# Performance work log

Measured on AMD Instinct MI355X. Metric: run time of the kernel, lower is better.

Reference implementation:

```python
import jax, jax.numpy as jnp
import numpy as np

EMBED_DIM = 1024
N_HEAD = 16
D_K = EMBED_DIM // N_HEAD


def setup_inputs() -> dict:
    key = jax.random.key(0)
    kq, kk, kv, kwq, kwk, kwv, kwo = jax.random.split(key, 7)
    B, S, E = 4, 2048, EMBED_DIM
    scale = 1.0 / np.sqrt(E)
    return {
        "Q": jax.random.normal(kq, (B, S, E), dtype=jnp.float32),
        "K": jax.random.normal(kk, (B, S, E), dtype=jnp.float32),
        "V": jax.random.normal(kv, (B, S, E), dtype=jnp.float32),
        "mask": jnp.zeros((1,), dtype=jnp.bool_),  # unused by the module's forward
        "Wq": jax.random.normal(kwq, (E, E), dtype=jnp.float32) * scale,
        "Wk": jax.random.normal(kwk, (E, E), dtype=jnp.float32) * scale,
        "Wv": jax.random.normal(kwv, (E, E), dtype=jnp.float32) * scale,
        "Wo": jax.random.normal(kwo, (E, E), dtype=jnp.float32) * scale,
    }


def reference(Q, K, V, mask, Wq, Wk, Wv, Wo):
    B, S, E = Q.shape
    H, Dk = N_HEAD, D_K
    # Linear projections (torch Linear: x @ W.T), split into heads -> [B,H,S,Dk]
    q = (Q @ Wq.T).reshape(B, S, H, Dk).transpose(0, 2, 1, 3)
    k = (K @ Wk.T).reshape(B, S, H, Dk).transpose(0, 2, 1, 3)
    v = (V @ Wv.T).reshape(B, S, H, Dk).transpose(0, 2, 1, 3)
    # Scaled dot-product attention (no mask is passed in the original forward;
    # dropout is identity in eval mode)
    scores = jnp.einsum("bhqd,bhkd->bhqk", q, k) / jnp.sqrt(jnp.float32(Dk))
    attn = jax.nn.softmax(scores, axis=-1)
    ctx = jnp.einsum("bhqk,bhkd->bhqd", attn, v)  # [B,H,S,Dk]
    ctx = ctx.transpose(0, 2, 1, 3).reshape(B, S, E)
    return ctx @ Wo.T
```

## Files before the change

kernel.cpp:

```cpp
#include <hip/hip_runtime.h>
#include <hip/hip_bf16.h>

#define B_  4
#define S_  2048
#define E_  1024
#define H_  16
#define DK_ 64
#define CSC 0.18033688011112042f

using bf16   = __bf16;
using bf16x8 = __attribute__((ext_vector_type(8))) __bf16;
using f32x4  = __attribute__((ext_vector_type(4))) float;

__device__ __forceinline__ f32x4 mfma16(bf16x8 a, bf16x8 b, f32x4 c) {
    return __builtin_amdgcn_mfma_f32_16x16x32_bf16(a, b, c, 0, 0, 0);
}

__device__ __forceinline__ bf16x8 cvt8(float4 a, float4 b) {
    bf16x8 r;
    r[0] = (bf16)a.x; r[1] = (bf16)a.y; r[2] = (bf16)a.z; r[3] = (bf16)a.w;
    r[4] = (bf16)b.x; r[5] = (bf16)b.y; r[6] = (bf16)b.z; r[7] = (bf16)b.w;
    return r;
}

__device__ __forceinline__ void gl16(const void* g, void* l) {
    __builtin_amdgcn_global_load_lds(
        (const __attribute__((address_space(1))) void*)g,
        (__attribute__((address_space(3))) void*)l, 16, 0, 0);
}

#define SBAR()  __builtin_amdgcn_s_barrier()
#define WV4()  { asm volatile("s_waitcnt vmcnt(4)" ::: "memory");   \
                 __builtin_amdgcn_sched_barrier(0); }
#define WL0()  { asm volatile("s_waitcnt lgkmcnt(0)" ::: "memory"); \
                 __builtin_amdgcn_sched_barrier(0); }

__global__ __launch_bounds__(256) void cvt_pair(const float* __restrict__ a,
                                                const float* __restrict__ b,
                                                bf16* __restrict__ da,
                                                bf16* __restrict__ db) {
    const float* s = blockIdx.y ? b : a;
    bf16* d = blockIdx.y ? db : da;
    const size_t i = (size_t)blockIdx.x * 256 + threadIdx.x;
    const float4 u = ((const float4*)s)[i * 2];
    const float4 v = ((const float4*)s)[i * 2 + 1];
    ((bf16x8*)d)[i] = cvt8(u, v);
}

__global__ __launch_bounds__(256) void cvtw3(const float* __restrict__ a,
                                             const float* __restrict__ b,
                                             const float* __restrict__ c,
                                             bf16* __restrict__ d, float s0) {
    const int y = blockIdx.y;
    const float* s = y == 0 ? a : y == 1 ? b : c;
    const float sc = y == 0 ? s0 : 1.f;
    const size_t i = (size_t)blockIdx.x * 256 + threadIdx.x;
    float4 u = ((const float4*)s)[i * 2];
    float4 v = ((const float4*)s)[i * 2 + 1];
    u.x *= sc; u.y *= sc; u.z *= sc; u.w *= sc;
    v.x *= sc; v.y *= sc; v.z *= sc; v.w *= sc;
    ((bf16x8*)(d + (size_t)y * E_ * E_))[i] = cvt8(u, v);
}

template <int MODE>
__global__ __launch_bounds__(512, 2) void gemm8(
    const bf16* __restrict__ Aq, const bf16* __restrict__ Ak,
    const bf16* __restrict__ Av, const bf16* __restrict__ Wb,
    bf16* __restrict__ qws, bf16* __restrict__ kws, bf16* __restrict__ vtws,
    float* __restrict__ fout, int selbase) {
    extern __shared__ __align__(16) char sm[];

    const int t = threadIdx.x;
    const int lane = t & 63, w = t >> 6;
    const int wm = w >> 2, wn = w & 3;
    const int quad = lane >> 4, l16 = lane & 15;

    int sel, gn;
    if (MODE == 0) {
        sel = selbase + (blockIdx.y >> 2);
        gn = (blockIdx.y & 3) * 256;
    } else {
        sel = 0;
        gn = blockIdx.y * 256;
    }
    const int gm = blockIdx.x * 256;

    const bf16* A = (MODE == 1) ? Aq : (sel == 0 ? Aq : sel == 1 ? Ak : Av);
    const bf16* W = (MODE == 1) ? Wb : Wb + (size_t)sel * E_ * E_;

    const int lr = lane >> 3;
    const int scw = (lane & 7) ^ lr;
    const int s0 = w * 2, s1 = s0 + 1;
    const int arow0 = (s0 >> 3) * 128 + (s0 & 7) * 8;
    const int arow1 = (s1 >> 3) * 128 + (s1 & 7) * 8;
    const int brow0 = (s0 >> 2) * 64 + (s0 & 3) * 8;
    const int brow1 = (s1 >> 2) * 64 + (s1 & 3) * 8;

    const char* gAa0 = (const char*)(A + (size_t)(gm + arow0 + lr) * E_) + scw * 16;
    const char* gAa1 = (const char*)(A + (size_t)(gm + arow1 + lr) * E_) + scw * 16;
    const char* gAb0 = gAa0 + (size_t)64 * E_ * 2;
    const char* gAb1 = gAa1 + (size_t)64 * E_ * 2;
    const char* gBa0 = (const char*)(W + (size_t)(gn + brow0 + lr) * E_) + scw * 16;
    const char* gBa1 = (const char*)(W + (size_t)(gn + brow1 + lr) * E_) + scw * 16;
    const char* gBb0 = gBa0 + (size_t)32 * E_ * 2;
    const char* gBb1 = gBa1 + (size_t)32 * E_ * 2;

#define STG_Aa(nb, kb) { gl16(gAa0 + (kb), sm + (nb) + arow0 * 128);              \
                         gl16(gAa1 + (kb), sm + (nb) + arow1 * 128); }
#define STG_Ab(nb, kb) { gl16(gAb0 + (kb), sm + (nb) + (arow0 + 64) * 128);       \
                         gl16(gAb1 + (kb), sm + (nb) + (arow1 + 64) * 128); }
#define STG_Ba(nb, kb) { gl16(gBa0 + (kb), sm + (nb) + 32768 + brow0 * 128);      \
                         gl16(gBa1 + (kb), sm + (nb) + 32768 + brow1 * 128); }
#define STG_Bb(nb, kb) { gl16(gBb0 + (kb), sm + (nb) + 32768 + (brow0+32) * 128); \
                         gl16(gBb1 + (kb), sm + (nb) + 32768 + (brow1+32) * 128); }

    const int cK0 = ((0 * 4 + quad) ^ (l16 & 7)) * 16;
    const int cK1 = ((1 * 4 + quad) ^ (l16 & 7)) * 16;

    f32x4 acc[8][4];
#pragma unroll
    for (int i = 0; i < 8; ++i)
#pragma unroll
        for (int j = 0; j < 4; ++j) acc[i][j] = f32x4{0.f, 0.f, 0.f, 0.f};

    bf16x8 Af[4][2], Bf[2][2];

#define LDA(cb, MH)                                                            \
    _Pragma("unroll") for (int ml = 0; ml < 4; ++ml) {                         \
        const int rb = (wm * 128 + (MH) * 64 + ml * 16 + l16) * 128;           \
        Af[ml][0] = *(const bf16x8*)(sm + (cb) + rb + cK0);                    \
        Af[ml][1] = *(const bf16x8*)(sm + (cb) + rb + cK1);                    \
    }
#define LDB(cb, NH)                                                            \
    _Pragma("unroll") for (int nl = 0; nl < 2; ++nl) {                         \
        const int rb = (wn * 64 + (NH) * 32 + nl * 16 + l16) * 128;            \
        Bf[nl][0] = *(const bf16x8*)(sm + (cb) + 32768 + rb + cK0);            \
        Bf[nl][1] = *(const bf16x8*)(sm + (cb) + 32768 + rb + cK1);            \
    }
#define MFMAQ(MH, NH)                                                          \
    __builtin_amdgcn_s_setprio(1);                                             \
    _Pragma("unroll") for (int ml = 0; ml < 4; ++ml)                           \
    _Pragma("unroll") for (int nl = 0; nl < 2; ++nl) {                         \
        acc[(MH)*4+ml][(NH)*2+nl] =                                            \
            mfma16(Af[ml][0], Bf[nl][0], acc[(MH)*4+ml][(NH)*2+nl]);           \
        acc[(MH)*4+ml][(NH)*2+nl] =                                            \
            mfma16(Af[ml][1], Bf[nl][1], acc[(MH)*4+ml][(NH)*2+nl]);           \
    }                                                                          \
    __builtin_amdgcn_s_setprio(0);

    STG_Aa(0, 0); STG_Ba(0, 0); STG_Bb(0, 0); STG_Ab(0, 0);
    WV4();
    SBAR();

    for (int kt = 0; kt < 16; ++kt) {
        const size_t cb = (size_t)(kt & 1) * 65536;
        const size_t nb = cb ^ 65536;
        const size_t kb = (size_t)(kt + 1 < 16 ? kt + 1 : 15) * 128;

        LDA(cb, 0); LDB(cb, 0);
        STG_Aa(nb, kb);
        WV4(); SBAR(); WL0();
        MFMAQ(0, 0);
        SBAR();

        LDB(cb, 1);
        STG_Ba(nb, kb);
        WV4(); SBAR(); WL0();
        MFMAQ(0, 1);
        SBAR();

        LDA(cb, 1);
        STG_Bb(nb, kb);
        SBAR(); WL0();
        MFMAQ(1, 1);
        SBAR();

        LDB(cb, 0);
        STG_Ab(nb, kb);
        WV4(); SBAR(); WL0();
        MFMAQ(1, 0);
        SBAR();
    }

#pragma unroll
    for (int mf = 0; mf < 8; ++mf)
#pragma unroll
        for (int nf = 0; nf < 4; ++nf) {
            const int col = gn + wn * 64 + nf * 16 + l16;
            const int row0 = gm + wm * 128 + mf * 16 + quad * 4;
            if (MODE == 1) {
#pragma unroll
                for (int r = 0; r < 4; ++r)
                    fout[(size_t)(row0 + r) * E_ + col] = acc[mf][nf][r];
            } else {
                const int h = col >> 6, d = col & (DK_ - 1);
#pragma unroll
                for (int r = 0; r < 4; ++r) {
                    const int i = row0 + r;
                    const int bb = i >> 11, s = i & (S_ - 1);
                    const float v = acc[mf][nf][r];
                    if (sel == 2)
                        vtws[(((size_t)(bb * H_ + h)) * DK_ + d) * S_ + s] = (bf16)v;
                    else if (sel == 1)
                        kws[(((size_t)(bb * H_ + h)) * S_ + s) * DK_ + d] = (bf16)v;
                    else
                        qws[(((size_t)(bb * H_ + h)) * S_ + s) * DK_ + d] = (bf16)v;
                }
            }
        }
#undef STG_Aa
#undef STG_Ab
#undef STG_Ba
#undef STG_Bb
#undef LDA
#undef LDB
#undef MFMAQ
}

#define PSTR 72
__global__ __launch_bounds__(256) void attn4(const bf16* __restrict__ q,
                                             const bf16* __restrict__ k,
                                             const bf16* __restrict__ vt,
                                             bf16* __restrict__ ctx) {
    __shared__ __align__(16) bf16 sK[64 * 64];
    __shared__ __align__(16) bf16 sV[64 * 64];
    __shared__ __align__(16) bf16 plds[4][32 * PSTR];

    const int t = threadIdx.x;
    const int lane = t & 63, wave = t >> 6;
    const int quad = lane >> 4, l16 = lane & 15;
    const int qb = (blockIdx.x * 4 + wave) * 32;
    const int bh = blockIdx.y;
    const size_t base  = (size_t)bh * S_ * DK_;
    const size_t baseT = (size_t)bh * DK_ * S_;
    bf16* pw = &plds[wave][0];

    const int srow = t >> 2, sc4 = (t & 3) * 16;
    const int cb = (t & 3) * 2, swr = srow & 7;
    const bf16* gK = k + base + (size_t)srow * DK_ + sc4;
    const bf16* gV = vt + baseT + (size_t)srow * S_ + sc4;
    char* wK0 = (char*)sK + srow * 128 + ((cb ^ swr) * 16);
    char* wK1 = (char*)sK + srow * 128 + (((cb + 1) ^ swr) * 16);
    char* wV0 = (char*)sV + srow * 128 + ((cb ^ swr) * 16);
    char* wV1 = (char*)sV + srow * 128 + (((cb + 1) ^ swr) * 16);

    bf16x8 rk[2], rv[2];
    rk[0] = *(const bf16x8*)(gK);
    rk[1] = *(const bf16x8*)(gK + 8);
    rv[0] = *(const bf16x8*)(gV);
    rv[1] = *(const bf16x8*)(gV + 8);

    bf16x8 aQ[2][2];
#pragma unroll
    for (int t2 = 0; t2 < 2; ++t2) {
        const bf16* qp = q + base + (size_t)(qb + t2 * 16 + l16) * DK_ + quad * 8;
        aQ[t2][0] = *(const bf16x8*)(qp);
        aQ[t2][1] = *(const bf16x8*)(qp + 32);
    }

    f32x4 acc[2][4];
    float l_i[2][4];
#pragma unroll
    for (int t2 = 0; t2 < 2; ++t2)
#pragma unroll
        for (int nb = 0; nb < 4; ++nb) {
            acc[t2][nb] = f32x4{0.f, 0.f, 0.f, 0.f};
            l_i[t2][nb] = 0.f;
        }

    for (int kt = 0; kt < S_ / 64; ++kt) {
        __syncthreads();
        *(bf16x8*)wK0 = rk[0];
        *(bf16x8*)wK1 = rk[1];
        *(bf16x8*)wV0 = rv[0];
        *(bf16x8*)wV1 = rv[1];
        __syncthreads();
        if (kt + 1 < S_ / 64) {
            const bf16* nK = gK + (size_t)(kt + 1) * 64 * DK_;
            const bf16* nV = gV + (size_t)(kt + 1) * 64;
            rk[0] = *(const bf16x8*)(nK);
            rk[1] = *(const bf16x8*)(nK + 8);
            rv[0] = *(const bf16x8*)(nV);
            rv[1] = *(const bf16x8*)(nV + 8);
        }

        f32x4 sc[2][4];
#pragma unroll
        for (int kb = 0; kb < 4; ++kb) {
            const int r = kb * 16 + l16, sw = r & 7;
            const bf16x8 b0 =
                *(const bf16x8*)((const char*)sK + r * 128 + ((quad ^ sw) * 16));
            const bf16x8 b1 = *(const bf16x8*)((const char*)sK + r * 128 +
                                               (((quad + 4) ^ sw) * 16));
#pragma unroll
            for (int t2 = 0; t2 < 2; ++t2) {
                f32x4 z = f32x4{0.f, 0.f, 0.f, 0.f};
                z = mfma16(aQ[t2][0], b0, z);
                sc[t2][kb] = mfma16(aQ[t2][1], b1, z);
            }
        }

#pragma unroll
        for (int t2 = 0; t2 < 2; ++t2)
#pragma unroll
            for (int r = 0; r < 4; ++r) {
                const int prow = (t2 * 16 + quad * 4 + r) * PSTR;
#pragma unroll
                for (int kb = 0; kb < 4; ++kb) {
                    const float p = __builtin_amdgcn_exp2f(sc[t2][kb][r]);
                    l_i[t2][r] += p;
                    pw[prow + kb * 16 + l16] = (bf16)p;
                }
            }

        bf16x8 aP[2][2];
#pragma unroll
        for (int t2 = 0; t2 < 2; ++t2) {
            aP[t2][0] = *(const bf16x8*)(pw + (t2 * 16 + l16) * PSTR + quad * 8);
            aP[t2][1] = *(const bf16x8*)(pw + (t2 * 16 + l16) * PSTR + 32 + quad * 8);
        }

#pragma unroll
        for (int nb = 0; nb < 4; ++nb) {
            const int r = nb * 16 + l16, sw = r & 7;
            const bf16x8 b0 =
                *(const bf16x8*)((const char*)sV + r * 128 + ((quad ^ sw) * 16));
            const bf16x8 b1 = *(const bf16x8*)((const char*)sV + r * 128 +
                                               (((quad + 4) ^ sw) * 16));
#pragma unroll
            for (int t2 = 0; t2 < 2; ++t2) {
                acc[t2][nb] = mfma16(aP[t2][0], b0, acc[t2][nb]);
                acc[t2][nb] = mfma16(aP[t2][1], b1, acc[t2][nb]);
            }
        }
    }

#pragma unroll
    for (int t2 = 0; t2 < 2; ++t2)
#pragma unroll
        for (int r = 0; r < 4; ++r) {
            float x = l_i[t2][r];
            x += __shfl_xor(x, 1);
            x += __shfl_xor(x, 2);
            x += __shfl_xor(x, 4);
            x += __shfl_xor(x, 8);
            l_i[t2][r] = 1.f / x;
        }

    const int b = bh >> 4, h = bh & (H_ - 1);
#pragma unroll
    for (int t2 = 0; t2 < 2; ++t2)
#pragma unroll
        for (int nb = 0; nb < 4; ++nb)
#pragma unroll
            for (int r = 0; r < 4; ++r) {
                const int s = qb + t2 * 16 + quad * 4 + r;
                const size_t idx =
                    ((size_t)(b * S_ + s)) * E_ + h * DK_ + nb * 16 + l16;
                ctx[idx] = (bf16)(acc[t2][nb][r] * l_i[t2][r]);
            }
}

extern "C" void kernel_launch(void* const* d_in, const int* in_sizes, int n_in,
                              void* d_out, int out_size, void* d_ws,
                              size_t ws_size, hipStream_t stream) {
    const float* Q  = (const float*)d_in[0];
    const float* K  = (const float*)d_in[1];
    const float* V  = (const float*)d_in[2];
    const float* Wq = (const float*)d_in[4];
    const float* Wk = (const float*)d_in[5];
    const float* Wv = (const float*)d_in[6];
    const float* Wo = (const float*)d_in[7];
    float* out = (float*)d_out;

    const size_t NTOK = (size_t)B_ * S_ * E_;
    bf16* qws  = (bf16*)d_ws;
    bf16* kws  = qws + NTOK;
    bf16* vtws = kws + NTOK;
    bf16* cws  = vtws + NTOK;

    bf16* wqkvb = cws;
    bf16* wob   = qws;
    bf16* Qb = (bf16*)d_out;
    bf16* Kb = Qb + NTOK;
    bf16* Vb = Qb;

    cvt_pair<<<dim3(4096, 2), 256, 0, stream>>>(Q, K, Qb, Kb);
    cvtw3<<<dim3(512, 3), 256, 0, stream>>>(Wq, Wk, Wv, wqkvb, CSC);

    gemm8<0><<<dim3(32, 8), 512, 131072, stream>>>(
        Qb, Kb, Vb, wqkvb, qws, kws, vtws, nullptr, 0);

    cvt_pair<<<dim3(4096, 1), 256, 0, stream>>>(V, V, Vb, Vb);

    gemm8<0><<<dim3(32, 4), 512, 131072, stream>>>(
        Qb, Kb, Vb, wqkvb, qws, kws, vtws, nullptr, 2);

    attn4<<<dim3(S_ / 128, B_ * H_), 256, 0, stream>>>(qws, kws, vtws, cws);

    cvtw3<<<dim3(512, 1), 256, 0, stream>>>(Wo, Wo, Wo, wob, 1.f);

    gemm8<1><<<dim3(32, 4), 512, 131072, stream>>>(
        cws, cws, cws, wob, nullptr, nullptr, nullptr, out, 0);
}
```

Baseline: 385.9 us.

## Rewrite projection GEMM as 128x256 tile with 4-stage K=32 pipeline

Replaces the 256x256 double-buffered GEMM (K-step 64, four quarter-MFMA phases with many barriers) with a 128x256 tile, a 4-stage ring buffer of K=32 slices in static shared memory, three slices in flight, and one barrier per step. The smaller tile doubles the grid (more blocks for the 256-CU part) and the deeper pipeline is meant to hide global-to-LDS latency with fewer sync points. The cost is lower arithmetic intensity per block, more global traffic for the weight operand, and a register/LDS footprint that changes occupancy.

```diff
diff --git a/kernel.cpp b/kernel.cpp
--- a/kernel.cpp
+++ b/kernel.cpp
@@ -29,11 +29,15 @@
         (__attribute__((address_space(3))) void*)l, 16, 0, 0);
 }
 
-#define SBAR()  __builtin_amdgcn_s_barrier()
-#define WV4()  { asm volatile("s_waitcnt vmcnt(4)" ::: "memory");   \
-                 __builtin_amdgcn_sched_barrier(0); }
-#define WL0()  { asm volatile("s_waitcnt lgkmcnt(0)" ::: "memory"); \
-                 __builtin_amdgcn_sched_barrier(0); }
+#define SBAR() __builtin_amdgcn_s_barrier()
+#define WV6() { asm volatile("s_waitcnt vmcnt(6)" ::: "memory");   \
+                __builtin_amdgcn_sched_barrier(0); }
+#define WV3() { asm volatile("s_waitcnt vmcnt(3)" ::: "memory");   \
+                __builtin_amdgcn_sched_barrier(0); }
+#define WV0() { asm volatile("s_waitcnt vmcnt(0)" ::: "memory");   \
+                __builtin_amdgcn_sched_barrier(0); }
+#define WL0() { asm volatile("s_waitcnt lgkmcnt(0)" ::: "memory"); \
+                __builtin_amdgcn_sched_barrier(0); }
 
 __global__ __launch_bounds__(256) void cvt_pair(const float* __restrict__ a,
                                                 const float* __restrict__ b,
@@ -63,12 +67,12 @@
 }
 
 template <int MODE>
-__global__ __launch_bounds__(512, 2) void gemm8(
+__global__ __launch_bounds__(512, 2) void gemmr(
     const bf16* __restrict__ Aq, const bf16* __restrict__ Ak,
     const bf16* __restrict__ Av, const bf16* __restrict__ Wb,
     bf16* __restrict__ qws, bf16* __restrict__ kws, bf16* __restrict__ vtws,
     float* __restrict__ fout, int selbase) {
-    extern __shared__ __align__(16) char sm[];
+    __shared__ __align__(16) char sm[4 * 24576];
 
     const int t = threadIdx.x;
     const int lane = t & 63, w = t >> 6;
@@ -83,122 +87,85 @@
         sel = 0;
         gn = blockIdx.y * 256;
     }
-    const int gm = blockIdx.x * 256;
+    const int gm = blockIdx.x * 128;
 
     const bf16* A = (MODE == 1) ? Aq : (sel == 0 ? Aq : sel == 1 ? Ak : Av);
     const bf16* W = (MODE == 1) ? Wb : Wb + (size_t)sel * E_ * E_;
 
-    const int lr = lane >> 3;
-    const int scw = (lane & 7) ^ lr;
-    const int s0 = w * 2, s1 = s0 + 1;
-    const int arow0 = (s0 >> 3) * 128 + (s0 & 7) * 8;
-    const int arow1 = (s1 >> 3) * 128 + (s1 & 7) * 8;
-    const int brow0 = (s0 >> 2) * 64 + (s0 & 3) * 8;
-    const int brow1 = (s1 >> 2) * 64 + (s1 & 3) * 8;
-
-    const char* gAa0 = (const char*)(A + (size_t)(gm + arow0 + lr) * E_) + scw * 16;
-    const char* gAa1 = (const char*)(A + (size_t)(gm + arow1 + lr) * E_) + scw * 16;
-    const char* gAb0 = gAa0 + (size_t)64 * E_ * 2;
-    const char* gAb1 = gAa1 + (size_t)64 * E_ * 2;
-    const char* gBa0 = (const char*)(W + (size_t)(gn + brow0 + lr) * E_) + scw * 16;
-    const char* gBa1 = (const char*)(W + (size_t)(gn + brow1 + lr) * E_) + scw * 16;
-    const char* gBb0 = gBa0 + (size_t)32 * E_ * 2;
-    const char* gBb1 = gBa1 + (size_t)32 * E_ * 2;
-
-#define STG_Aa(nb, kb) { gl16(gAa0 + (kb), sm + (nb) + arow0 * 128);              \
-                         gl16(gAa1 + (kb), sm + (nb) + arow1 * 128); }
-#define STG_Ab(nb, kb) { gl16(gAb0 + (kb), sm + (nb) + (arow0 + 64) * 128);       \
-                         gl16(gAb1 + (kb), sm + (nb) + (arow1 + 64) * 128); }
-#define STG_Ba(nb, kb) { gl16(gBa0 + (kb), sm + (nb) + 32768 + brow0 * 128);      \
-                         gl16(gBa1 + (kb), sm + (nb) + 32768 + brow1 * 128); }
-#define STG_Bb(nb, kb) { gl16(gBb0 + (kb), sm + (nb) + 32768 + (brow0+32) * 128); \
-                         gl16(gBb1 + (kb), sm + (nb) + 32768 + (brow1+32) * 128); }
-
-    const int cK0 = ((0 * 4 + quad) ^ (l16 & 7)) * 16;
-    const int cK1 = ((1 * 4 + quad) ^ (l16 & 7)) * 16;
-
-    f32x4 acc[8][4];
-#pragma unroll
-    for (int i = 0; i < 8; ++i)
+    const int srow = lane >> 2;
+    const int scw  = (lane & 3) ^ ((lane >> 3) & 3);
+    const char* gA  = (const char*)(A + (size_t)(gm + w * 16 + srow) * E_) + scw * 16;
+    const char* gB0 = (const char*)(W + (size_t)(gn + w * 32 + srow) * E_) + scw * 16;
+    const char* gB1 = gB0 + (size_t)16 * E_ * 2;
+
+#define STG(s) {                                                       \
+        const int _b = ((s) & 3) * 24576;                              \
+        const size_t _k = (size_t)(s) * 64;         \
+        gl16(gA + _k, sm + _b + w * 1024);                             \
+        gl16(gB0 + _k, sm + _b + 8192 + w * 2048);                     \
+        gl16(gB1 + _k, sm + _b + 8192 + w * 2048 + 1024);              \
+    }
+
+    bf16x8 Af[4], Bf[4];
+#define LDFRAGS(s) {                                                   \
+        const int _b = ((s) & 3) * 24576;                              \
+        _Pragma("unroll") for (int ms = 0; ms < 4; ++ms) {             \
+            const int r = wm * 64 + ms * 16 + l16;                     \
+            Af[ms] = *(const bf16x8*)(sm + _b + r * 64 +               \
+                                      ((quad ^ ((r >> 1) & 3)) * 16)); \
+        }                                                              \
+        _Pragma("unroll") for (int ns = 0; ns < 4; ++ns) {             \
+            const int r = wn * 64 + ns * 16 + l16;                     \
+            Bf[ns] = *(const bf16x8*)(sm + _b + 8192 + r * 64 +        \
+                                      ((quad ^ ((r >> 1) & 3)) * 16)); \
+        }                                                              \
+    }
+
+#define MFMACL() {                                                     \
+        __builtin_amdgcn_s_setprio(1);                                 \
+        _Pragma("unroll") for (int ms = 0; ms < 4; ++ms)               \
+        _Pragma("unroll") for (int ns = 0; ns < 4; ++ns)               \
+            acc[ms][ns] = mfma16(Af[ms], Bf[ns], acc[ms][ns]);         \
+        __builtin_amdgcn_s_setprio(0);                                 \
+    }
+
+    f32x4 acc[4][4];
+#pragma unroll
+    for (int i = 0; i < 4; ++i)
 #pragma unroll
         for (int j = 0; j < 4; ++j) acc[i][j] = f32x4{0.f, 0.f, 0.f, 0.f};
 
-    bf16x8 Af[4][2], Bf[2][2];
-
-#define LDA(cb, MH)                                                            \
-    _Pragma("unroll") for (int ml = 0; ml < 4; ++ml) {                         \
-        const int rb = (wm * 128 + (MH) * 64 + ml * 16 + l16) * 128;           \
-        Af[ml][0] = *(const bf16x8*)(sm + (cb) + rb + cK0);                    \
-        Af[ml][1] = *(const bf16x8*)(sm + (cb) + rb + cK1);                    \
-    }
-#define LDB(cb, NH)                                                            \
-    _Pragma("unroll") for (int nl = 0; nl < 2; ++nl) {                         \
-        const int rb = (wn * 64 + (NH) * 32 + nl * 16 + l16) * 128;            \
-        Bf[nl][0] = *(const bf16x8*)(sm + (cb) + 32768 + rb + cK0);            \
-        Bf[nl][1] = *(const bf16x8*)(sm + (cb) + 32768 + rb + cK1);            \
-    }
-#define MFMAQ(MH, NH)                                                          \
-    __builtin_amdgcn_s_setprio(1);                                             \
-    _Pragma("unroll") for (int ml = 0; ml < 4; ++ml)                           \
-    _Pragma("unroll") for (int nl = 0; nl < 2; ++nl) {                         \
-        acc[(MH)*4+ml][(NH)*2+nl] =                                            \
-            mfma16(Af[ml][0], Bf[nl][0], acc[(MH)*4+ml][(NH)*2+nl]);           \
-        acc[(MH)*4+ml][(NH)*2+nl] =                                            \
-            mfma16(Af[ml][1], Bf[nl][1], acc[(MH)*4+ml][(NH)*2+nl]);           \
-    }                                                                          \
-    __builtin_amdgcn_s_setprio(0);
-
-    STG_Aa(0, 0); STG_Ba(0, 0); STG_Bb(0, 0); STG_Ab(0, 0);
-    WV4();
-    SBAR();
-
-    for (int kt = 0; kt < 16; ++kt) {
-        const size_t cb = (size_t)(kt & 1) * 65536;
-        const size_t nb = cb ^ 65536;
-        const size_t kb = (size_t)(kt + 1 < 16 ? kt + 1 : 15) * 128;
-
-        LDA(cb, 0); LDB(cb, 0);
-        STG_Aa(nb, kb);
-        WV4(); SBAR(); WL0();
-        MFMAQ(0, 0);
+    STG(0); STG(1); STG(2);
+
+    for (int s = 0; s < 29; ++s) {
+        WV6();
         SBAR();
-
-        LDB(cb, 1);
-        STG_Ba(nb, kb);
-        WV4(); SBAR(); WL0();
-        MFMAQ(0, 1);
-        SBAR();
-
-        LDA(cb, 1);
-        STG_Bb(nb, kb);
-        SBAR(); WL0();
-        MFMAQ(1, 1);
-        SBAR();
-
-        LDB(cb, 0);
-        STG_Ab(nb, kb);
-        WV4(); SBAR(); WL0();
-        MFMAQ(1, 0);
-        SBAR();
-    }
-
-#pragma unroll
-    for (int mf = 0; mf < 8; ++mf)
-#pragma unroll
-        for (int nf = 0; nf < 4; ++nf) {
-            const int col = gn + wn * 64 + nf * 16 + l16;
-            const int row0 = gm + wm * 128 + mf * 16 + quad * 4;
+        STG(s + 3);
+        LDFRAGS(s);
+        WL0();
+        MFMACL();
+    }
+    WV6(); SBAR(); LDFRAGS(29); WL0(); MFMACL();
+    WV3(); SBAR(); LDFRAGS(30); WL0(); MFMACL();
+    WV0(); SBAR(); LDFRAGS(31); WL0(); MFMACL();
+
+#pragma unroll
+    for (int ms = 0; ms < 4; ++ms)
+#pragma unroll
+        for (int ns = 0; ns < 4; ++ns) {
+            const int col = gn + wn * 64 + ns * 16 + l16;
+            const int row0 = gm + wm * 64 + ms * 16 + quad * 4;
             if (MODE == 1) {
 #pragma unroll
                 for (int r = 0; r < 4; ++r)
-                    fout[(size_t)(row0 + r) * E_ + col] = acc[mf][nf][r];
+                    fout[(size_t)(row0 + r) * E_ + col] = acc[ms][ns][r];
             } else {
                 const int h = col >> 6, d = col & (DK_ - 1);
 #pragma unroll
                 for (int r = 0; r < 4; ++r) {
                     const int i = row0 + r;
                     const int bb = i >> 11, s = i & (S_ - 1);
-                    const float v = acc[mf][nf][r];
+                    const float v = acc[ms][ns][r];
                     if (sel == 2)
                         vtws[(((size_t)(bb * H_ + h)) * DK_ + d) * S_ + s] = (bf16)v;
                     else if (sel == 1)
@@ -208,13 +175,9 @@
                 }
             }
         }
-#undef STG_Aa
-#undef STG_Ab
-#undef STG_Ba
-#undef STG_Bb
-#undef LDA
-#undef LDB
-#undef MFMAQ
+#undef STG
+#undef LDFRAGS
+#undef MFMACL
 }
 
 #define PSTR 72
@@ -388,18 +351,18 @@
     cvt_pair<<<dim3(4096, 2), 256, 0, stream>>>(Q, K, Qb, Kb);
     cvtw3<<<dim3(512, 3), 256, 0, stream>>>(Wq, Wk, Wv, wqkvb, CSC);
 
-    gemm8<0><<<dim3(32, 8), 512, 131072, stream>>>(
+    gemmr<0><<<dim3(64, 8), 512, 0, stream>>>(
         Qb, Kb, Vb, wqkvb, qws, kws, vtws, nullptr, 0);
 
     cvt_pair<<<dim3(4096, 1), 256, 0, stream>>>(V, V, Vb, Vb);
 
-    gemm8<0><<<dim3(32, 4), 512, 131072, stream>>>(
+    gemmr<0><<<dim3(64, 4), 512, 0, stream>>>(
         Qb, Kb, Vb, wqkvb, qws, kws, vtws, nullptr, 2);
 
     attn4<<<dim3(S_ / 128, B_ * H_), 256, 0, stream>>>(qws, kws, vtws, cws);
 
     cvtw3<<<dim3(512, 1), 256, 0, stream>>>(Wo, Wo, Wo, wob, 1.f);
 
-    gemm8<1><<<dim3(32, 4), 512, 131072, stream>>>(
+    gemmr<1><<<dim3(64, 4), 512, 0, stream>>>(
         cws, cws, cws, wob, nullptr, nullptr, nullptr, out, 0);
 }
```

Result: no change. 384.4 us (-0.4%).
